# Kernel optimization log

Hardware: AMD Instinct MI355X
Metric: run time of the kernel (lower is better)

## Reference

```python
import jax, jax.numpy as jnp
import numpy as np

CTX_WIN = 5
PAD = (CTX_WIN - 1) // 2


def setup_inputs() -> dict:
    key = jax.random.key(0)
    k1, k2, k3 = jax.random.split(key, 3)
    B, S, H, A = 64, 1024, 128, 8
    return {
        "batch_docIn": jax.random.normal(k1, (B, S, H), dtype=jnp.float32),
        "aspEmbed_weight": jax.random.uniform(k2, (A, CTX_WIN * H), dtype=jnp.float32, minval=-0.01, maxval=0.01),
        "aspProj": jax.random.uniform(k3, (A, H, H), dtype=jnp.float32, minval=-0.01, maxval=0.01),
    }


def reference(batch_docIn, aspEmbed_weight, aspProj):
    B, S, H = batch_docIn.shape
    A = aspProj.shape[0]
    # Per-aspect projection: (A, B, S, H)
    proj = jnp.einsum('bsh,ahf->absf', batch_docIn, aspProj)
    E = aspEmbed_weight.reshape(A, H, CTX_WIN)
    # Zero-pad along seq, then accumulate windowed scores without materializing
    padded = jnp.pad(proj, ((0, 0), (0, 0), (PAD, PAD), (0, 0)))
    attn = sum(
        jnp.einsum('absh,ah->abs',
                   jax.lax.dynamic_slice_in_dim(padded, w, S, axis=2),
                   E[:, :, w])
        for w in range(CTX_WIN)
    )  # (A, B, S)
    attn = jax.nn.softmax(attn, axis=2)  # softmax over seq (torch dim=1)
    rep = jnp.einsum('absh,abs->abh', proj, attn)  # (A, B, H)
    # outputs: attn (B, A, S), rep (B, A, H)
    return attn.transpose(1, 0, 2), rep.transpose(1, 0, 2)
```

## Files before the change

### kernel.cpp

```cpp
#include <hip/hip_runtime.h>
#include <hip/hip_bf16.h>

#define S_DIM 1024
#define H_DIM 128
#define A_DIM 8
#define W_WIN 5

typedef unsigned int uint;
typedef unsigned short ushort;
typedef __attribute__((ext_vector_type(8))) short short8;
typedef __attribute__((ext_vector_type(4))) float f32x4;

union U128 { uint4 u; short8 s; };

__device__ __forceinline__ ushort f2bf(float f) {
    uint u = __float_as_uint(f);
    uint r = (u + 0x7fffu + ((u >> 16) & 1u)) >> 16;
    return (ushort)r;
}

__global__ __launch_bounds__(128) void k_g(const float* __restrict__ P,
                                           const float* __restrict__ We,
                                           ushort* __restrict__ Gt,
                                           float* __restrict__ Z, int nZ) {
    const int a = blockIdx.x;
    const int h = threadIdx.x;
    if (a >= A_DIM) {
        for (int i = h; i < W_WIN * H_DIM; i += 128) Gt[a * (W_WIN * H_DIM) + i] = 0;
        if (a == A_DIM) for (int i = h; i < nZ; i += 128) Z[i] = 0.f;
        return;
    }
    __shared__ float Es[H_DIM * W_WIN];
    for (int i = h; i < H_DIM * W_WIN; i += 128) Es[i] = We[a * (H_DIM * W_WIN) + i];
    __syncthreads();

    const float* Pr = P + ((size_t)a * H_DIM + h) * H_DIM;
    float acc[W_WIN] = {0.f, 0.f, 0.f, 0.f, 0.f};
#pragma unroll 8
    for (int f = 0; f < H_DIM; f += 4) {
        float4 pv = *(const float4*)(Pr + f);
        float pj[4] = {pv.x, pv.y, pv.z, pv.w};
#pragma unroll
        for (int j = 0; j < 4; ++j) {
            const float p = pj[j];
            const float* e = &Es[(f + j) * W_WIN];
#pragma unroll
            for (int w = 0; w < W_WIN; ++w) acc[w] += p * e[w];
        }
    }
#pragma unroll
    for (int w = 0; w < W_WIN; ++w)
        Gt[a * (W_WIN * H_DIM) + w * H_DIM + h] = f2bf(acc[w]);
}

#define CS 128
#define RROWS (CS + 4)
#define GPAD 81
__global__ __launch_bounds__(256) void k_scores(const float* __restrict__ Din,
                                                const ushort* __restrict__ Gt,
                                                float* __restrict__ score,
                                                float* __restrict__ Z) {
    __shared__ uint4 Dl[RROWS * 16];
    __shared__ uint4 Gl[16 * GPAD];
    __shared__ float Zl[8];
    const int b  = blockIdx.y;
    const int s0 = blockIdx.x * CS;
    const int t  = threadIdx.x;
    const float* Db = Din + (size_t)b * S_DIM * H_DIM;

    for (int i = t; i < RROWS * 16; i += 256) {
        const int r = i >> 4, c = i & 15;
        const int gs = s0 - 2 + r;
        float4 va = make_float4(0.f, 0.f, 0.f, 0.f), vb = va;
        if (gs >= 0 && gs < S_DIM) {
            const float* p = Db + (size_t)gs * H_DIM + c * 8;
            va = ((const float4*)p)[0];
            vb = ((const float4*)p)[1];
        }
        uint4 q;
        q.x = (uint)f2bf(va.x) | ((uint)f2bf(va.y) << 16);
        q.y = (uint)f2bf(va.z) | ((uint)f2bf(va.w) << 16);
        q.z = (uint)f2bf(vb.x) | ((uint)f2bf(vb.y) << 16);
        q.w = (uint)f2bf(vb.z) | ((uint)f2bf(vb.w) << 16);
        Dl[r * 16 + (c ^ (r & 15))] = q;
    }
    {
        const uint4* Gg = (const uint4*)Gt;
        for (int i = t; i < 16 * 80; i += 256) {
            const int n = i / 80, c = i - n * 80;
            Gl[n * GPAD + c] = Gg[i];
        }
    }
    if (t < 8) Zl[t] = 0.f;
    __syncthreads();

    const int lane = t & 63;
    const int wv   = t >> 6;
    const int lm   = lane & 15;
    const int lq   = lane >> 4;

    f32x4 acc0 = {0.f, 0.f, 0.f, 0.f};
    f32x4 acc1 = {0.f, 0.f, 0.f, 0.f};
#pragma unroll
    for (int kk = 0; kk < 20; ++kk) {
        const int w = kk >> 2;
        const int r0 = wv * 16 + lm + w;
        const int cidx = (kk & 3) * 4 + lq;
        const int cx = cidx ^ (r0 & 15);
        U128 av0, av1, bv;
        bv.u  = Gl[lm * GPAD + kk * 4 + lq];
        av0.u = Dl[r0 * 16 + cx];
        av1.u = Dl[(r0 + 64) * 16 + cx];
        acc0 = __builtin_amdgcn_mfma_f32_16x16x32_bf16(av0.s, bv.s, acc0, 0, 0, 0);
        acc1 = __builtin_amdgcn_mfma_f32_16x16x32_bf16(av1.s, bv.s, acc1, 0, 0, 0);
    }

    const int n = lm;
    if (n < A_DIM) {
        float* op = score + (((size_t)b * A_DIM + n) * S_DIM) + s0 + wv * 16 + lq * 4;
        *(f32x4*)op = acc0;
        *(f32x4*)(op + 64) = acc1;
    }

    float es = __expf(acc0.x) + __expf(acc0.y) + __expf(acc0.z) + __expf(acc0.w)
             + __expf(acc1.x) + __expf(acc1.y) + __expf(acc1.z) + __expf(acc1.w);
    es += __shfl_xor(es, 16);
    es += __shfl_xor(es, 32);
    if ((lane & 48) == 0 && lm < A_DIM) atomicAdd(&Zl[lm], es);
    __syncthreads();
    if (t < A_DIM) atomicAdd(&Z[b * A_DIM + t], Zl[t]);
}

__global__ __launch_bounds__(256) void k_wsum(const float* __restrict__ Din,
                                              const float* __restrict__ score,
                                              const float* __restrict__ Z,
                                              float* __restrict__ attn,
                                              float* __restrict__ wsP) {
    __shared__ float el[A_DIM * 128];
    const int slc = blockIdx.x;
    const int b = blockIdx.y;
    const int t = threadIdx.x;

    {
        const int a = t >> 5, s4 = (t & 31) << 2;
        const float rz = 1.0f / Z[b * A_DIM + a];
        const size_t off = ((size_t)b * A_DIM + a) * S_DIM + slc * 128 + s4;
        float4 v = *(const float4*)(score + off);
        float4 e;
        e.x = __expf(v.x) * rz; e.y = __expf(v.y) * rz;
        e.z = __expf(v.z) * rz; e.w = __expf(v.w) * rz;
        *(float4*)(attn + off) = e;
        *(float4*)(&el[a * 128 + s4]) = e;
    }
    __syncthreads();

    const int h = t & 127;
    const int half = __builtin_amdgcn_readfirstlane(t >> 7);
    const int s0 = slc * 128 + half * 64;

    const float* dp = Din + ((size_t)b * S_DIM + s0) * H_DIM + h;
    float dreg[64];
#pragma unroll
    for (int i = 0; i < 64; ++i) dreg[i] = dp[(size_t)i * H_DIM];

    float* wp = wsP + ((size_t)(b * 16 + slc * 2 + half) * A_DIM) * H_DIM + h;
#pragma unroll
    for (int a = 0; a < A_DIM; ++a) {
        const float* aa = &el[a * 128 + half * 64];
        float acc = 0.f;
#pragma unroll
        for (int i = 0; i < 64; ++i) acc += aa[i] * dreg[i];
        wp[(size_t)a * H_DIM] = acc;
    }
}

__global__ __launch_bounds__(128) void k_rep(const float* __restrict__ wsP,
                                             const float* __restrict__ P,
                                             float* __restrict__ rep) {
    __shared__ float ws[H_DIM];
    const int ba = blockIdx.x;
    const int b = ba >> 3, a = ba & 7;
    const int t = threadIdx.x;
    float s = 0.f;
#pragma unroll
    for (int k = 0; k < 16; ++k)
        s += wsP[(((size_t)(b * 16 + k)) * A_DIM + a) * H_DIM + t];
    ws[t] = s;
    __syncthreads();
    const float* Pa = P + (size_t)a * H_DIM * H_DIM + t;
    float acc = 0.f;
#pragma unroll 32
    for (int hh = 0; hh < H_DIM; ++hh)
        acc += ws[hh] * Pa[(size_t)hh * H_DIM];
    rep[(size_t)ba * H_DIM + t] = acc;
}

extern "C" void kernel_launch(void* const* d_in, const int* in_sizes, int n_in,
                              void* d_out, int out_size, void* d_ws, size_t ws_size,
                              hipStream_t stream) {
    const float* docIn = (const float*)d_in[0];
    const float* We    = (const float*)d_in[1];
    const float* P     = (const float*)d_in[2];
    float* out = (float*)d_out;

    const int B = in_sizes[0] / (S_DIM * H_DIM);

    ushort* Gt   = (ushort*)d_ws;
    float* Z     = (float*)((char*)d_ws + 24576);
    float* score = (float*)((char*)d_ws + 32768);
    float* wsP   = score + (size_t)B * A_DIM * S_DIM;

    k_g<<<16, 128, 0, stream>>>(P, We, Gt, Z, B * A_DIM);
    k_scores<<<dim3(S_DIM / CS, B), 256, 0, stream>>>(docIn, Gt, score, Z);
    k_wsum<<<dim3(S_DIM / 128, B), 256, 0, stream>>>(docIn, score, Z, out, wsP);
    k_rep<<<B * A_DIM, 128, 0, stream>>>(wsP, P, out + (size_t)B * A_DIM * S_DIM);
}
```

Measured before the change: 96.50 us.

## Fuse softmax-weighted sum into score kernel using MFMA and partial sums

Folds the weighted-sum stage into the score kernel. Exponentiated scores are staged in LDS as bf16 and multiplied against the already-loaded bf16 input tile with MFMA, so the second full read of the input is gone. Atomics on Z are replaced by per-slice partial sums that a final kernel reduces while it normalises attn and computes rep. This drops one kernel launch and one pass over the 32MB input, at the cost of bf16 precision in the weighted sum and scattered 2-byte LDS gathers to build the B fragments.

```diff
diff --git a/kernel.cpp b/kernel.cpp
--- a/kernel.cpp
+++ b/kernel.cpp
@@ -21,13 +21,11 @@
 
 __global__ __launch_bounds__(128) void k_g(const float* __restrict__ P,
                                            const float* __restrict__ We,
-                                           ushort* __restrict__ Gt,
-                                           float* __restrict__ Z, int nZ) {
+                                           ushort* __restrict__ Gt) {
     const int a = blockIdx.x;
     const int h = threadIdx.x;
     if (a >= A_DIM) {
         for (int i = h; i < W_WIN * H_DIM; i += 128) Gt[a * (W_WIN * H_DIM) + i] = 0;
-        if (a == A_DIM) for (int i = h; i < nZ; i += 128) Z[i] = 0.f;
         return;
     }
     __shared__ float Es[H_DIM * W_WIN];
@@ -56,16 +54,20 @@
 #define CS 128
 #define RROWS (CS + 4)
 #define GPAD 81
+#define EPITCH 136
 __global__ __launch_bounds__(256) void k_scores(const float* __restrict__ Din,
                                                 const ushort* __restrict__ Gt,
-                                                float* __restrict__ score,
-                                                float* __restrict__ Z) {
+                                                float* __restrict__ escore,
+                                                float* __restrict__ numPart,
+                                                float* __restrict__ Zpart) {
     __shared__ uint4 Dl[RROWS * 16];
     __shared__ uint4 Gl[16 * GPAD];
-    __shared__ float Zl[8];
-    const int b  = blockIdx.y;
-    const int s0 = blockIdx.x * CS;
-    const int t  = threadIdx.x;
+    __shared__ ushort el[16 * EPITCH];
+    __shared__ float Zw[32];
+    const int b   = blockIdx.y;
+    const int slc = blockIdx.x;
+    const int s0  = slc * CS;
+    const int t   = threadIdx.x;
     const float* Db = Din + (size_t)b * S_DIM * H_DIM;
 
     for (int i = t; i < RROWS * 16; i += 256) {
@@ -91,7 +93,6 @@
             Gl[n * GPAD + c] = Gg[i];
         }
     }
-    if (t < 8) Zl[t] = 0.f;
     __syncthreads();
 
     const int lane = t & 63;
@@ -115,78 +116,103 @@
         acc1 = __builtin_amdgcn_mfma_f32_16x16x32_bf16(av1.s, bv.s, acc1, 0, 0, 0);
     }
 
-    const int n = lm;
-    if (n < A_DIM) {
-        float* op = score + (((size_t)b * A_DIM + n) * S_DIM) + s0 + wv * 16 + lq * 4;
-        *(f32x4*)op = acc0;
-        *(f32x4*)(op + 64) = acc1;
-    }
-
-    float es = __expf(acc0.x) + __expf(acc0.y) + __expf(acc0.z) + __expf(acc0.w)
-             + __expf(acc1.x) + __expf(acc1.y) + __expf(acc1.z) + __expf(acc1.w);
+    float4 e0, e1;
+    e0.x = __expf(acc0.x); e0.y = __expf(acc0.y); e0.z = __expf(acc0.z); e0.w = __expf(acc0.w);
+    e1.x = __expf(acc1.x); e1.y = __expf(acc1.y); e1.z = __expf(acc1.z); e1.w = __expf(acc1.w);
+
+    if (lm < A_DIM) {
+        float* op = escore + (((size_t)b * A_DIM + lm) * S_DIM) + s0 + wv * 16 + lq * 4;
+        *(float4*)op = e0;
+        *(float4*)(op + 64) = e1;
+    }
+    {
+        const int sb = wv * 16 + lq * 4;
+        uint2 d0, d1;
+        d0.x = (uint)f2bf(e0.x) | ((uint)f2bf(e0.y) << 16);
+        d0.y = (uint)f2bf(e0.z) | ((uint)f2bf(e0.w) << 16);
+        d1.x = (uint)f2bf(e1.x) | ((uint)f2bf(e1.y) << 16);
+        d1.y = (uint)f2bf(e1.z) | ((uint)f2bf(e1.w) << 16);
+        *(uint2*)(&el[lm * EPITCH + sb])      = d0;
+        *(uint2*)(&el[lm * EPITCH + sb + 64]) = d1;
+    }
+    float es = e0.x + e0.y + e0.z + e0.w + e1.x + e1.y + e1.z + e1.w;
     es += __shfl_xor(es, 16);
     es += __shfl_xor(es, 32);
-    if ((lane & 48) == 0 && lm < A_DIM) atomicAdd(&Zl[lm], es);
-    __syncthreads();
-    if (t < A_DIM) atomicAdd(&Z[b * A_DIM + t], Zl[t]);
-}
-
-__global__ __launch_bounds__(256) void k_wsum(const float* __restrict__ Din,
-                                              const float* __restrict__ score,
-                                              const float* __restrict__ Z,
-                                              float* __restrict__ attn,
-                                              float* __restrict__ wsP) {
-    __shared__ float el[A_DIM * 128];
-    const int slc = blockIdx.x;
-    const int b = blockIdx.y;
-    const int t = threadIdx.x;
-
-    {
-        const int a = t >> 5, s4 = (t & 31) << 2;
-        const float rz = 1.0f / Z[b * A_DIM + a];
-        const size_t off = ((size_t)b * A_DIM + a) * S_DIM + slc * 128 + s4;
-        float4 v = *(const float4*)(score + off);
-        float4 e;
-        e.x = __expf(v.x) * rz; e.y = __expf(v.y) * rz;
-        e.z = __expf(v.z) * rz; e.w = __expf(v.w) * rz;
-        *(float4*)(attn + off) = e;
-        *(float4*)(&el[a * 128 + s4]) = e;
-    }
-    __syncthreads();
-
-    const int h = t & 127;
-    const int half = __builtin_amdgcn_readfirstlane(t >> 7);
-    const int s0 = slc * 128 + half * 64;
-
-    const float* dp = Din + ((size_t)b * S_DIM + s0) * H_DIM + h;
-    float dreg[64];
-#pragma unroll
-    for (int i = 0; i < 64; ++i) dreg[i] = dp[(size_t)i * H_DIM];
-
-    float* wp = wsP + ((size_t)(b * 16 + slc * 2 + half) * A_DIM) * H_DIM + h;
-#pragma unroll
-    for (int a = 0; a < A_DIM; ++a) {
-        const float* aa = &el[a * 128 + half * 64];
-        float acc = 0.f;
-#pragma unroll
-        for (int i = 0; i < 64; ++i) acc += aa[i] * dreg[i];
-        wp[(size_t)a * H_DIM] = acc;
-    }
-}
-
-__global__ __launch_bounds__(128) void k_rep(const float* __restrict__ wsP,
-                                             const float* __restrict__ P,
-                                             float* __restrict__ rep) {
+    if (lq == 0 && lm < A_DIM) Zw[wv * 8 + lm] = es;
+    __syncthreads();
+
+    const ushort* Dls = (const ushort*)Dl;
+    U128 afr[4];
+#pragma unroll
+    for (int kk = 0; kk < 4; ++kk)
+        afr[kk].u = *(const uint4*)(&el[lm * EPITCH + kk * 32 + lq * 8]);
+
+    f32x4 accN[2] = {{0.f,0.f,0.f,0.f},{0.f,0.f,0.f,0.f}};
+#pragma unroll
+    for (int nt = 0; nt < 2; ++nt) {
+        const int h  = (wv * 2 + nt) * 16 + lm;
+        const int ch = h >> 3, hw = h & 7;
+#pragma unroll
+        for (int kk = 0; kk < 4; ++kk) {
+            uint p[4];
+#pragma unroll
+            for (int jj = 0; jj < 4; ++jj) {
+                const int sj = kk * 32 + lq * 8 + jj * 2;
+                const int ra = sj + 2, rb = sj + 3;
+                const uint lo = Dls[(ra * 16 + (ch ^ (ra & 15))) * 8 + hw];
+                const uint hi = Dls[(rb * 16 + (ch ^ (rb & 15))) * 8 + hw];
+                p[jj] = lo | (hi << 16);
+            }
+            U128 bfr; bfr.u = make_uint4(p[0], p[1], p[2], p[3]);
+            accN[nt] = __builtin_amdgcn_mfma_f32_16x16x32_bf16(afr[kk].s, bfr.s, accN[nt], 0, 0, 0);
+        }
+    }
+
+    if (lq < 2) {
+#pragma unroll
+        for (int nt = 0; nt < 2; ++nt) {
+            const int h = (wv * 2 + nt) * 16 + lm;
+#pragma unroll
+            for (int r = 0; r < 4; ++r)
+                numPart[(((size_t)(b * 8 + slc) * 8) + lq * 4 + r) * H_DIM + h] = accN[nt][r];
+        }
+    }
+    if (t < A_DIM)
+        Zpart[(b * 8 + slc) * 8 + t] = Zw[t] + Zw[8 + t] + Zw[16 + t] + Zw[24 + t];
+}
+
+__global__ __launch_bounds__(128) void k_final(const float* __restrict__ escore,
+                                               const float* __restrict__ numPart,
+                                               const float* __restrict__ Zpart,
+                                               const float* __restrict__ P,
+                                               float* __restrict__ attn,
+                                               float* __restrict__ rep) {
     __shared__ float ws[H_DIM];
     const int ba = blockIdx.x;
     const int b = ba >> 3, a = ba & 7;
     const int t = threadIdx.x;
+
+    float Zs = 0.f;
+#pragma unroll
+    for (int k = 0; k < 8; ++k) Zs += Zpart[(b * 8 + k) * 8 + a];
+    const float rz = 1.0f / Zs;
+
     float s = 0.f;
 #pragma unroll
-    for (int k = 0; k < 16; ++k)
-        s += wsP[(((size_t)(b * 16 + k)) * A_DIM + a) * H_DIM + t];
-    ws[t] = s;
-    __syncthreads();
+    for (int k = 0; k < 8; ++k)
+        s += numPart[(((size_t)(b * 8 + k) * 8) + a) * H_DIM + t];
+    ws[t] = s * rz;
+
+    const float* ep = escore + (size_t)ba * S_DIM;
+    float* ap = attn + (size_t)ba * S_DIM;
+#pragma unroll
+    for (int i = 0; i < 2; ++i) {
+        float4 v = *(const float4*)(ep + i * 512 + t * 4);
+        v.x *= rz; v.y *= rz; v.z *= rz; v.w *= rz;
+        *(float4*)(ap + i * 512 + t * 4) = v;
+    }
+    __syncthreads();
+
     const float* Pa = P + (size_t)a * H_DIM * H_DIM + t;
     float acc = 0.f;
 #pragma unroll 32
@@ -205,13 +231,13 @@
 
     const int B = in_sizes[0] / (S_DIM * H_DIM);
 
-    ushort* Gt   = (ushort*)d_ws;
-    float* Z     = (float*)((char*)d_ws + 24576);
-    float* score = (float*)((char*)d_ws + 32768);
-    float* wsP   = score + (size_t)B * A_DIM * S_DIM;
-
-    k_g<<<16, 128, 0, stream>>>(P, We, Gt, Z, B * A_DIM);
-    k_scores<<<dim3(S_DIM / CS, B), 256, 0, stream>>>(docIn, Gt, score, Z);
-    k_wsum<<<dim3(S_DIM / 128, B), 256, 0, stream>>>(docIn, score, Z, out, wsP);
-    k_rep<<<B * A_DIM, 128, 0, stream>>>(wsP, P, out + (size_t)B * A_DIM * S_DIM);
-}
+    ushort* Gt     = (ushort*)d_ws;
+    float* escore  = (float*)((char*)d_ws + 32768);
+    float* numPart = escore + (size_t)B * A_DIM * S_DIM;
+    float* Zpart   = numPart + (size_t)B * 8 * A_DIM * H_DIM;
+
+    k_g<<<16, 128, 0, stream>>>(P, We, Gt);
+    k_scores<<<dim3(S_DIM / CS, B), 256, 0, stream>>>(docIn, Gt, escore, numPart, Zpart);
+    k_final<<<B * A_DIM, 128, 0, stream>>>(escore, numPart, Zpart, P, out,
+                                           out + (size_t)B * A_DIM * S_DIM);
+}
```

Result: faster. 91.94 us (-4.7%).
